# Performance work log

Hardware: AMD Instinct MI355X
Metric: run time of the kernel (lower is better)

Reference implementation:

```python
import jax, jax.numpy as jnp
import numpy as np

NP_, NB_, E_, BE_ = 10000, 30000, 300000, 8192
PIN, BIN, EA = 128, 128, 16
HID, GH = 64, 4
D, TH, L, NC, SEQ = 128, 4, 2, 10, 6


def _ln(x, g, b, eps=1e-5):
    m = x.mean(-1, keepdims=True)
    v = ((x - m) ** 2).mean(-1, keepdims=True)
    return (x - m) * jax.lax.rsqrt(v + eps) * g + b


def _seg_softmax(e, seg, n):
    m = jax.ops.segment_max(e, seg, num_segments=n)
    m = jnp.where(jnp.isfinite(m), m, 0.0)
    ex = jnp.exp(e - m[seg])
    s = jax.ops.segment_sum(ex, seg, num_segments=n)
    return ex / (s[seg] + 1e-16)


def _gatv2(xs, xd, es, ed, ea, Wl, bl, Wr, br, We, att, bias, n_dst):
    # PyG GATv2Conv, concat=False, add_self_loops=False, eval mode (no dropout)
    xl = (xs @ Wl + bl).reshape(-1, GH, HID)   # [Ns,H,C] source transform (message content)
    xr = (xd @ Wr + br).reshape(-1, GH, HID)   # [Nd,H,C] dest transform
    eh = (ea @ We).reshape(-1, GH, HID)        # [E,H,C] edge transform (no bias in PyG)
    msg = xl[es] + xr[ed] + eh                 # [E,H,C]
    score = jnp.einsum('ehc,hc->eh', jax.nn.leaky_relu(msg, 0.2), att)
    alpha = _seg_softmax(score, ed, n_dst)     # softmax over in-edges per dest node
    out = jax.ops.segment_sum(alpha[..., None] * xl[es], ed, num_segments=n_dst)
    return out.mean(axis=1) + bias             # concat=False -> mean over heads


def _mha(x, Wqkv, bqkv, Wo, bo):
    S, d = x.shape
    dh = d // TH
    q, k, v = jnp.split(x @ Wqkv + bqkv, 3, axis=-1)
    q = q.reshape(S, TH, dh).transpose(1, 0, 2)
    k = k.reshape(S, TH, dh).transpose(1, 0, 2)
    v = v.reshape(S, TH, dh).transpose(1, 0, 2)
    a = jax.nn.softmax(jnp.einsum('hqd,hkd->hqk', q, k) / jnp.sqrt(jnp.float32(dh)), axis=-1)
    o = jnp.einsum('hqk,hkd->hqd', a, v).transpose(1, 0, 2).reshape(S, d)
    return o @ Wo + bo


def _forward(pitcher_feat, batter_feat, edge_attr, history_states,
             Wp, bp, Wb, bb,
             rel_Wl, rel_bl, rel_Wr, rel_br, rel_We, rel_att, rel_bias,
             rev_Wl, rev_bl, rev_Wr, rev_br, rev_We, rev_att, rev_bias,
             Wgs, bgs, Wet, bet, pos,
             Wqkv, bqkv, Wo, bo, ln1g, ln1b, W1, b1, W2, b2, ln2g, ln2b,
             Wc1, bc1, Wc2, bc2,
             edge_src, edge_dst, edge_ids):
    gelu = lambda t: jax.nn.gelu(t, approximate=False)
    px = gelu(pitcher_feat @ Wp + bp)
    bx = gelu(batter_feat @ Wb + bb)
    # ('pitcher','faces','batter'): messages pitcher->batter, aggregated at batter nodes
    h_b = gelu(_gatv2(px, bx, edge_src, edge_dst, edge_attr,
                      rel_Wl, rel_bl, rel_Wr, rel_br, rel_We, rel_att, rel_bias, bx.shape[0]))
    # reversed relation: batter->pitcher, aggregated at pitcher nodes
    h_p = gelu(_gatv2(bx, px, edge_dst, edge_src, edge_attr,
                      rev_Wl, rev_bl, rev_Wr, rev_br, rev_We, rev_att, rev_bias, px.shape[0]))
    state = jnp.concatenate([h_p.mean(0), h_b.mean(0), edge_attr.mean(0)], -1) @ Wgs + bgs
    tok = jnp.concatenate([h_p[edge_src[edge_ids]], h_b[edge_dst[edge_ids]],
                           edge_attr[edge_ids]], -1) @ Wet + bet
    x = jnp.concatenate([history_states, state[None]], 0) + pos[:SEQ]
    for i in range(L):  # post-LN TransformerEncoderLayer, gelu activation, eval (no dropout)
        x = _ln(x + _mha(x, Wqkv[i], bqkv[i], Wo[i], bo[i]), ln1g[i], ln1b[i])
        f = gelu(x @ W1[i] + b1[i]) @ W2[i] + b2[i]
        x = _ln(x + f, ln2g[i], ln2b[i])
    ctx = x[-1]
    cat = jnp.concatenate([tok, jnp.broadcast_to(ctx, (tok.shape[0], D))], -1)
    return gelu(cat @ Wc1 + bc1) @ Wc2 + bc2


def setup_inputs() -> dict:
    key = jax.random.key(0)
    ks = iter(jax.random.split(key, 64))
    nrm = lambda shape, s: jax.random.normal(next(ks), shape, dtype=jnp.float32) * s
    d = {
        'pitcher_feat': nrm((NP_, PIN), 1.0),
        'batter_feat': nrm((NB_, BIN), 1.0),
        'edge_attr': nrm((E_, EA), 1.0),
        'history_states': nrm((SEQ - 1, D), 1.0),
        'Wp': nrm((PIN, HID), 0.05), 'bp': jnp.zeros((HID,), jnp.float32),
        'Wb': nrm((BIN, HID), 0.05), 'bb': jnp.zeros((HID,), jnp.float32),
    }
    for p in ('rel', 'rev'):
        d[p + '_Wl'] = nrm((HID, GH * HID), 0.05)
        d[p + '_bl'] = jnp.zeros((GH * HID,), jnp.float32)
        d[p + '_Wr'] = nrm((HID, GH * HID), 0.05)
        d[p + '_br'] = jnp.zeros((GH * HID,), jnp.float32)
        d[p + '_We'] = nrm((EA, GH * HID), 0.05)
        d[p + '_att'] = nrm((GH, HID), 0.05)
        d[p + '_bias'] = jnp.zeros((HID,), jnp.float32)
    cin = 2 * HID + EA
    d['Wgs'] = nrm((cin, D), 0.05); d['bgs'] = jnp.zeros((D,), jnp.float32)
    d['Wet'] = nrm((cin, D), 0.05); d['bet'] = jnp.zeros((D,), jnp.float32)
    d['pos'] = nrm((SEQ, D), 0.02)
    d['Wqkv'] = nrm((L, D, 3 * D), 0.05); d['bqkv'] = jnp.zeros((L, 3 * D), jnp.float32)
    d['Wo'] = nrm((L, D, D), 0.05); d['bo'] = jnp.zeros((L, D), jnp.float32)
    d['ln1g'] = jnp.ones((L, D), jnp.float32); d['ln1b'] = jnp.zeros((L, D), jnp.float32)
    d['W1'] = nrm((L, D, 4 * D), 0.05); d['b1'] = jnp.zeros((L, 4 * D), jnp.float32)
    d['W2'] = nrm((L, 4 * D, D), 0.05); d['b2'] = jnp.zeros((L, D), jnp.float32)
    d['ln2g'] = jnp.ones((L, D), jnp.float32); d['ln2b'] = jnp.zeros((L, D), jnp.float32)
    d['Wc1'] = nrm((2 * D, D), 0.05); d['bc1'] = jnp.zeros((D,), jnp.float32)
    d['Wc2'] = nrm((D, NC), 0.05); d['bc2'] = jnp.zeros((NC,), jnp.float32)
    d['edge_src'] = jax.random.randint(next(ks), (E_,), 0, NP_)
    d['edge_dst'] = jax.random.randint(next(ks), (E_,), 0, NB_)
    d['edge_ids'] = jax.random.randint(next(ks), (BE_,), 0, E_)
    return d


def reference(pitcher_feat, batter_feat, edge_attr, history_states,
              Wp, bp, Wb, bb,
              rel_Wl, rel_bl, rel_Wr, rel_br, rel_We, rel_att, rel_bias,
              rev_Wl, rev_bl, rev_Wr, rev_br, rev_We, rev_att, rev_bias,
              Wgs, bgs, Wet, bet, pos,
              Wqkv, bqkv, Wo, bo, ln1g, ln1b, W1, b1, W2, b2, ln2g, ln2b,
              Wc1, bc1, Wc2, bc2,
              edge_src, edge_dst, edge_ids):
    return _forward(pitcher_feat, batter_feat, edge_attr, history_states,
                    Wp, bp, Wb, bb,
                    rel_Wl, rel_bl, rel_Wr, rel_br, rel_We, rel_att, rel_bias,
                    rev_Wl, rev_bl, rev_Wr, rev_br, rev_We, rev_att, rev_bias,
                    Wgs, bgs, Wet, bet, pos,
                    Wqkv, bqkv, Wo, bo, ln1g, ln1b, W1, b1, W2, b2, ln2g, ln2b,
                    Wc1, bc1, Wc2, bc2,
                    edge_src, edge_dst, edge_ids)
```

## Files before the change

kernel.cpp:

```cpp
#include <hip/hip_runtime.h>
#include <math.h>

#define NP 10000
#define NB 30000
#define NEDGE 300000
#define BEDGE 8192
#define EAD 16
#define HID 64
#define GH 4
#define CW 256
#define DD 128
#define SEQ 6
#define NCLS 10
#define L 2

__device__ __forceinline__ float geluf(float x){
  return 0.5f * x * (1.0f + erff(x * 0.7071067811865475f));
}

__device__ __forceinline__ float b2f(unsigned short u){
  unsigned v = ((unsigned)u) << 16;
  return __int_as_float(v);
}
__device__ __forceinline__ unsigned short f2b(float f){
  unsigned x = __float_as_uint(f);
  unsigned r = x + 0x7FFF + ((x >> 16) & 1);
  return (unsigned short)(r >> 16);
}

typedef __attribute__((ext_vector_type(8))) short bf16x8;
typedef __attribute__((ext_vector_type(4))) float f32x4;

template<int KQ, int NTILES, bool A_F32, bool GELU>
__device__ __forceinline__
void mfma_gemm_body(int bid, const void* __restrict__ Av, const float* __restrict__ W,
                    const float* __restrict__ bias, unsigned short* __restrict__ out,
                    int M, unsigned short* __restrict__ sWt)
{
  constexpr int N  = NTILES * 16;
  constexpr int KP = KQ + 8;
  int t = threadIdx.x, w = t >> 6, l = t & 63;
  int c = l & 15, g = l >> 4;
  for (int idx = t; idx < KQ*N; idx += 256){
    int k = idx / N, n = idx - k*N;
    sWt[n*KP + k] = f2b(W[idx]);
  }
  __syncthreads();
  int rowbase = bid*64 + w*16;
  int arow = rowbase + c; if (arow > M-1) arow = M-1;
  f32x4 acc[NTILES] = {};
  #pragma unroll
  for (int ks = 0; ks < KQ/32; ++ks){
    int koff = ks*32 + g*8;
    bf16x8 a;
    if constexpr (A_F32){
      const float* Af = (const float*)Av + (size_t)arow*KQ + koff;
      float4 f0 = *(const float4*)Af;
      float4 f1 = *(const float4*)(Af + 4);
      a[0]=(short)f2b(f0.x); a[1]=(short)f2b(f0.y); a[2]=(short)f2b(f0.z); a[3]=(short)f2b(f0.w);
      a[4]=(short)f2b(f1.x); a[5]=(short)f2b(f1.y); a[6]=(short)f2b(f1.z); a[7]=(short)f2b(f1.w);
    } else {
      a = *(const bf16x8*)((const unsigned short*)Av + (size_t)arow*KQ + koff);
    }
    #pragma unroll
    for (int nt = 0; nt < NTILES; ++nt){
      bf16x8 b = *(const bf16x8*)&sWt[(nt*16 + c)*KP + koff];
      acc[nt] = __builtin_amdgcn_mfma_f32_16x16x32_bf16(a, b, acc[nt], 0, 0, 0);
    }
  }
  #pragma unroll
  for (int nt = 0; nt < NTILES; ++nt){
    #pragma unroll
    for (int j = 0; j < 4; ++j){
      int row = rowbase + g*4 + j;
      if (row < M){
        int col = nt*16 + c;
        float v = acc[nt][j] + bias[col];
        if (GELU) v = geluf(v);
        out[(size_t)row*N + col] = f2b(v);
      }
    }
  }
}

__global__ __launch_bounds__(256)
void k1_count_enc(const int* __restrict__ edst, const int* __restrict__ esrc,
                  int* __restrict__ degA, int* __restrict__ degB,
                  const float* __restrict__ pit, const float* __restrict__ Wp,
                  const float* __restrict__ bp, unsigned short* __restrict__ px,
                  const float* __restrict__ bat, const float* __restrict__ Wb,
                  const float* __restrict__ bb, unsigned short* __restrict__ bx,
                  int nbCount, int nbP)
{
  __shared__ unsigned short sWt[64*136];
  int b = blockIdx.x;
  if (b < nbCount){
    int i = b*256 + threadIdx.x;
    if (i < NEDGE){
      atomicAdd(&degA[edst[i]], 1);
      atomicAdd(&degB[esrc[i]], 1);
    }
  } else if (b < nbCount + nbP){
    mfma_gemm_body<128,4,true,true>(b - nbCount, pit, Wp, bp, px, NP, sWt);
  } else {
    mfma_gemm_body<128,4,true,true>(b - nbCount - nbP, bat, Wb, bb, bx, NB, sWt);
  }
}

__device__ void scan_dev(const int* __restrict__ deg, int* __restrict__ row_start,
                         int* __restrict__ cursor, int n){
  __shared__ int wsum[16];
  __shared__ int sbase;
  int t = threadIdx.x, w = t >> 6, l = t & 63;
  if (t == 0) sbase = 0;
  __syncthreads();
  for (int base = 0; base < n; base += 4096){
    int i = base + t*4;
    int4 v = make_int4(0,0,0,0);
    if (i < n) v = *(const int4*)(deg + i);
    int tsum = v.x + v.y + v.z + v.w;
    int x = tsum;
    #pragma unroll
    for (int off = 1; off < 64; off <<= 1){
      int y = __shfl_up(x, off);
      if (l >= off) x += y;
    }
    if (l == 63) wsum[w] = x;
    __syncthreads();
    int woff = 0, tot = 0;
    #pragma unroll
    for (int ww = 0; ww < 16; ++ww){
      int wv = wsum[ww];
      if (ww < w) woff += wv;
      tot += wv;
    }
    int excl = sbase + woff + x - tsum;
    if (i < n){
      int e1 = excl + v.x, e2 = excl + v.x + v.y, e3 = excl + v.x + v.y + v.z;
      row_start[i]   = excl; cursor[i]   = excl;
      row_start[i+1] = e1;   cursor[i+1] = e1;
      row_start[i+2] = e2;   cursor[i+2] = e2;
      row_start[i+3] = e3;   cursor[i+3] = e3;
    }
    __syncthreads();
    if (t == 0) sbase += tot;
    __syncthreads();
  }
  if (t == 0) row_start[n] = sbase;
}

__global__ __launch_bounds__(1024)
void scan2_kernel(const int* __restrict__ degA, int* __restrict__ rsA, int* __restrict__ curA, int nA,
                  const int* __restrict__ degB, int* __restrict__ rsB, int* __restrict__ curB, int nB,
                  float* __restrict__ mvec){
  if (blockIdx.x == 0){
    scan_dev(degA, rsA, curA, nA);
  } else {
    if (threadIdx.x < 144) mvec[threadIdx.x] = 0.f;
    scan_dev(degB, rsB, curB, nB);
  }
}

__global__ __launch_bounds__(256)
void k2_scatter_proj(const int* __restrict__ edst, const int* __restrict__ esrc,
                     int* __restrict__ curA, int* __restrict__ curB,
                     int2* __restrict__ csrA, int2* __restrict__ csrB,
                     const unsigned short* __restrict__ px, const unsigned short* __restrict__ bx,
                     const float* __restrict__ rel_Wl, const float* __restrict__ rel_bl,
                     const float* __restrict__ rel_Wr, const float* __restrict__ rel_br,
                     const float* __restrict__ rev_Wl, const float* __restrict__ rev_bl,
                     const float* __restrict__ rev_Wr, const float* __restrict__ rev_br,
                     unsigned short* __restrict__ xlA, unsigned short* __restrict__ xrA,
                     unsigned short* __restrict__ xlB, unsigned short* __restrict__ xrB,
                     int nbScat, int nbP, int nbB)
{
  __shared__ unsigned short sWt[256*72];
  int b = blockIdx.x;
  if (b < nbScat){
    int i = b*256 + threadIdx.x;
    if (i < NEDGE){
      int d = edst[i], s = esrc[i];
      int p = atomicAdd(&curA[d], 1);
      csrA[p] = make_int2(i, s);
      int q = atomicAdd(&curB[s], 1);
      csrB[q] = make_int2(i, d);
    }
  } else {
    b -= nbScat;
    if (b < nbP)               mfma_gemm_body<64,16,false,false>(b,            px, rel_Wl, rel_bl, xlA, NP, sWt);
    else if (b < nbP + nbB)    mfma_gemm_body<64,16,false,false>(b-nbP,        bx, rel_Wr, rel_br, xrA, NB, sWt);
    else if (b < nbP + 2*nbB)  mfma_gemm_body<64,16,false,false>(b-nbP-nbB,    bx, rev_Wl, rev_bl, xlB, NB, sWt);
    else                       mfma_gemm_body<64,16,false,false>(b-nbP-2*nbB,  px, rev_Wr, rev_br, xrB, NP, sWt);
  }
}

#define GAT_PAIR(X0, X1, EV0, EV1, V1OK, P0MASK)                             \
  {                                                                          \
    float x0 = b2f(X0.x), x1 = b2f(X0.y), x2 = b2f(X0.z), x3 = b2f(X0.w);    \
    float y0 = b2f(X1.x), y1 = b2f(X1.y), y2 = b2f(X1.z), y3 = b2f(X1.w);    \
    float h00 = x0 + r0, h01 = x1 + r1, h02 = x2 + r2, h03 = x3 + r3;        \
    float h10 = y0 + r0, h11 = y1 + r1, h12 = y2 + r2, h13 = y3 + r3;        \
    int ia0 = __float_as_int(EV0);                                           \
    int ia1 = __float_as_int(EV1);                                           \
    _Pragma("unroll")                                                        \
    for (int k = 0; k < EAD; ++k){                                           \
      float c0 = __int_as_float(__builtin_amdgcn_readlane(ia0, k));          \
      float c1 = __int_as_float(__builtin_amdgcn_readlane(ia1, k));          \
      float4 wv = *(const float4*)&sWe[k*CW + 4*l];                          \
      h00 = fmaf(c0, wv.x, h00); h01 = fmaf(c0, wv.y, h01);                  \
      h02 = fmaf(c0, wv.z, h02); h03 = fmaf(c0, wv.w, h03);                  \
      h10 = fmaf(c1, wv.x, h10); h11 = fmaf(c1, wv.y, h11);                  \
      h12 = fmaf(c1, wv.z, h12); h13 = fmaf(c1, wv.w, h13);                  \
    }                                                                        \
    h00 = (h00 > 0.f ? h00 : 0.2f*h00) * at.x;                               \
    h01 = (h01 > 0.f ? h01 : 0.2f*h01) * at.y;                               \
    h02 = (h02 > 0.f ? h02 : 0.2f*h02) * at.z;                               \
    h03 = (h03 > 0.f ? h03 : 0.2f*h03) * at.w;                               \
    h10 = (h10 > 0.f ? h10 : 0.2f*h10) * at.x;                               \
    h11 = (h11 > 0.f ? h11 : 0.2f*h11) * at.y;                               \
    h12 = (h12 > 0.f ? h12 : 0.2f*h12) * at.z;                               \
    h13 = (h13 > 0.f ? h13 : 0.2f*h13) * at.w;                               \
    float g0 = (h00 + h01) + (h02 + h03);                                    \
    float g1 = (h10 + h11) + (h12 + h13);                                    \
    _Pragma("unroll")                                                        \
    for (int off = 1; off < 16; off <<= 1){                                  \
      g0 += __shfl_xor(g0, off);                                             \
      g1 += __shfl_xor(g1, off);                                             \
    }                                                                        \
    float gm = (V1OK) ? fmaxf(g0, g1) : g0;                                  \
    float mn = fmaxf(m, gm);                                                 \
    float cc = __expf(m - mn);                                               \
    float p0 = __expf(g0 - mn);                                              \
    if (!(P0MASK)) p0 = 0.f;                                                 \
    float p1 = (V1OK) ? __expf(g1 - mn) : 0.f;                               \
    s  = fmaf(s, cc, p0 + p1);                                               \
    a0 = fmaf(a0, cc, fmaf(p1, y0, p0*x0));                                  \
    a1 = fmaf(a1, cc, fmaf(p1, y1, p0*x1));                                  \
    a2 = fmaf(a2, cc, fmaf(p1, y2, p0*x2));                                  \
    a3 = fmaf(a3, cc, fmaf(p1, y3, p0*x3));                                  \
    m = mn;                                                                  \
  }

__global__ __launch_bounds__(256)
void gat2_kernel(const unsigned short* __restrict__ xlA_, const unsigned short* __restrict__ xrA_,
                 const float* __restrict__ WeA, const float* __restrict__ attA,
                 const float* __restrict__ biasA, const int2* __restrict__ csrA_,
                 const int* __restrict__ rsA_, float* __restrict__ houtA,
                 const unsigned short* __restrict__ xlB_, const unsigned short* __restrict__ xrB_,
                 const float* __restrict__ WeB, const float* __restrict__ attB,
                 const float* __restrict__ biasB, const int2* __restrict__ csrB_,
                 const int* __restrict__ rsB_, float* __restrict__ houtB,
                 const float* __restrict__ ea, int gsplit)
{
  __shared__ float sWe[16*CW];
  bool isA = (int)blockIdx.x < gsplit;
  const unsigned short* xl = isA ? xlA_ : xlB_;
  const unsigned short* xr = isA ? xrA_ : xrB_;
  const float* We   = isA ? WeA   : WeB;
  const float* att  = isA ? attA  : attB;
  const float* bias = isA ? biasA : biasB;
  const int2* csr   = isA ? csrA_ : csrB_;
  const int* row_start = isA ? rsA_ : rsB_;
  float* hout = isA ? houtA : houtB;
  int ndst = isA ? NB : NP;
  int bid  = isA ? (int)blockIdx.x : (int)blockIdx.x - gsplit;
  int nblk = isA ? gsplit : (int)gridDim.x - gsplit;

  int t = threadIdx.x, l = t & 63;
  for (int i = t*4; i < 16*CW; i += 1024)
    *(float4*)&sWe[i] = *(const float4*)&We[i];
  __syncthreads();
  float4 at = *(const float4*)&att[4*l];
  float4 bi = *(const float4*)&bias[(l & 15)*4];
  int wid = bid*4 + (t >> 6);
  int nw = nblk*4;
  for (int d = wid; d < ndst; d += nw){
    ushort4 ru = *(const ushort4*)(xr + (size_t)d*CW + 4*l);
    float r0 = b2f(ru.x), r1 = b2f(ru.y), r2 = b2f(ru.z), r3 = b2f(ru.w);
    int rs = row_start[d], re = row_start[d+1];
    float m = -INFINITY, s = 0.f;
    float a0 = 0.f, a1 = 0.f, a2 = 0.f, a3 = 0.f;
    if (rs < re){
      int last = re - 1;
      #define CLMP(x) ((x) > last ? last : (x))
      int2 qA0 = csr[rs],         qA1 = csr[CLMP(rs+1)];
      int2 qB0 = csr[CLMP(rs+2)], qB1 = csr[CLMP(rs+3)];
      int2 nA0 = csr[CLMP(rs+4)], nA1 = csr[CLMP(rs+5)];
      int2 nB0 = csr[CLMP(rs+6)], nB1 = csr[CLMP(rs+7)];
      ushort4 xA0 = *(const ushort4*)(xl + (size_t)qA0.y*CW + 4*l);
      ushort4 xA1 = *(const ushort4*)(xl + (size_t)qA1.y*CW + 4*l);
      float  evA0 = ea[(size_t)qA0.x*EAD + (l & 15)];
      float  evA1 = ea[(size_t)qA1.x*EAD + (l & 15)];
      ushort4 xB0 = *(const ushort4*)(xl + (size_t)qB0.y*CW + 4*l);
      ushort4 xB1 = *(const ushort4*)(xl + (size_t)qB1.y*CW + 4*l);
      float  evB0 = ea[(size_t)qB0.x*EAD + (l & 15)];
      float  evB1 = ea[(size_t)qB1.x*EAD + (l & 15)];
      for (int i = rs; i < re; i += 4){
        int2 mA0 = csr[CLMP(i+8)],  mA1 = csr[CLMP(i+9)];
        int2 mB0 = csr[CLMP(i+10)], mB1 = csr[CLMP(i+11)];
        GAT_PAIR(xA0, xA1, evA0, evA1, (i+1 < re), true);
        xA0 = *(const ushort4*)(xl + (size_t)nA0.y*CW + 4*l);
        xA1 = *(const ushort4*)(xl + (size_t)nA1.y*CW + 4*l);
        evA0 = ea[(size_t)nA0.x*EAD + (l & 15)];
        evA1 = ea[(size_t)nA1.x*EAD + (l & 15)];
        nA0 = mA0; nA1 = mA1;
        GAT_PAIR(xB0, xB1, evB0, evB1, (i+3 < re), (i+2 < re));
        xB0 = *(const ushort4*)(xl + (size_t)nB0.y*CW + 4*l);
        xB1 = *(const ushort4*)(xl + (size_t)nB1.y*CW + 4*l);
        evB0 = ea[(size_t)nB0.x*EAD + (l & 15)];
        evB1 = ea[(size_t)nB1.x*EAD + (l & 15)];
        nB0 = mB0; nB1 = mB1;
      }
      #undef CLMP
    }
    float inv = 1.f / (s + 1e-16f);
    float v0 = a0*inv, v1 = a1*inv, v2 = a2*inv, v3 = a3*inv;
    v0 += __shfl_xor(v0, 16); v1 += __shfl_xor(v1, 16);
    v2 += __shfl_xor(v2, 16); v3 += __shfl_xor(v3, 16);
    v0 += __shfl_xor(v0, 32); v1 += __shfl_xor(v1, 32);
    v2 += __shfl_xor(v2, 32); v3 += __shfl_xor(v3, 32);
    if (l < 16){
      float4 o;
      o.x = geluf(v0*0.25f + bi.x);
      o.y = geluf(v1*0.25f + bi.y);
      o.z = geluf(v2*0.25f + bi.z);
      o.w = geluf(v3*0.25f + bi.w);
      *(float4*)(hout + (size_t)d*HID + 4*l) = o;
    }
  }
}

__device__ __forceinline__ void colsum_seg(int bid, int nb, const float4* __restrict__ in4,
                                           long total4, int n4, float* __restrict__ out,
                                           float scale, float* lds){
  int t = threadIdx.x, l = t & 63, w = t >> 6;
  long gid = (long)bid*256 + t;
  long stride = (long)nb*256;
  float4 acc = make_float4(0.f,0.f,0.f,0.f);
  for (long i = gid; i < total4; i += stride){
    float4 v = in4[i];
    acc.x += v.x; acc.y += v.y; acc.z += v.z; acc.w += v.w;
  }
  for (int off = n4; off < 64; off <<= 1){
    acc.x += __shfl_xor(acc.x, off);
    acc.y += __shfl_xor(acc.y, off);
    acc.z += __shfl_xor(acc.z, off);
    acc.w += __shfl_xor(acc.w, off);
  }
  if (l < n4) *(float4*)&lds[(w*n4 + l)*4] = acc;
  __syncthreads();
  if (t < n4*4){
    float sum = lds[t] + lds[n4*4 + t] + lds[2*n4*4 + t] + lds[3*n4*4 + t];
    atomicAdd(&out[t], sum * scale);
  }
  __syncthreads();
}

__device__ void colsum3_body(int bid, int nb, const float* __restrict__ hp,
                             const float* __restrict__ hb, const float* __restrict__ ea,
                             float* __restrict__ mvec){
  __shared__ float lds[4*16*4];
  colsum_seg(bid, nb, (const float4*)ea, (long)NEDGE*EAD/4, 4,  mvec+128, 1.f/NEDGE, lds);
  colsum_seg(bid, nb, (const float4*)hb, (long)NB*HID/4,    16, mvec+64,  1.f/NB,    lds);
  colsum_seg(bid, nb, (const float4*)hp, (long)NP*HID/4,    16, mvec,     1.f/NP,    lds);
}

__device__ void gemmcat_body(int bid, const float* __restrict__ hp, const float* __restrict__ hb,
                             const float* __restrict__ ea, const int* __restrict__ esrc,
                             const int* __restrict__ edst, const int* __restrict__ eids,
                             const float* __restrict__ W, const float* __restrict__ bias,
                             float* __restrict__ out)
{
  __shared__ float sAT[16][68];
  __shared__ float sB[16][68];
  __shared__ int sS[64], sD[64], sE[64];
  int t = threadIdx.x;
  int m0 = (bid >> 1)*64, n0 = (bid & 1)*64;
  if (t < 64){
    int e = eids[m0 + t];
    sS[t] = esrc[e]; sD[t] = edst[e]; sE[t] = e;
  }
  __syncthreads();
  int tr = t >> 4, tc = t & 15;
  float acc[4][4] = {};
  for (int k0 = 0; k0 < 144; k0 += 16){
    {
      int r = t >> 2, c = (t & 3) * 4;
      const float* src; int col = k0 + c;
      if (k0 < 64)       { src = hp + (size_t)sS[r]*HID; }
      else if (k0 < 128) { src = hb + (size_t)sD[r]*HID; col -= 64; }
      else               { src = ea + (size_t)sE[r]*EAD; col -= 128; }
      float4 va = *(const float4*)(src + col);
      sAT[c+0][r] = va.x; sAT[c+1][r] = va.y; sAT[c+2][r] = va.z; sAT[c+3][r] = va.w;
    }
    {
      int r = t >> 4, c = (t & 15) * 4;
      float4 vb = *(const float4*)(W + (size_t)(k0+r)*DD + n0 + c);
      *(float4*)&sB[r][c] = vb;
    }
    __syncthreads();
    #pragma unroll
    for (int k = 0; k < 16; ++k){
      float4 av = *(const float4*)&sAT[k][tr*4];
      float4 bv = *(const float4*)&sB[k][tc*4];
      acc[0][0] = fmaf(av.x, bv.x, acc[0][0]);
      acc[0][1] = fmaf(av.x, bv.y, acc[0][1]);
      acc[0][2] = fmaf(av.x, bv.z, acc[0][2]);
      acc[0][3] = fmaf(av.x, bv.w, acc[0][3]);
      acc[1][0] = fmaf(av.y, bv.x, acc[1][0]);
      acc[1][1] = fmaf(av.y, bv.y, acc[1][1]);
      acc[1][2] = fmaf(av.y, bv.z, acc[1][2]);
      acc[1][3] = fmaf(av.y, bv.w, acc[1][3]);
      acc[2][0] = fmaf(av.z, bv.x, acc[2][0]);
      acc[2][1] = fmaf(av.z, bv.y, acc[2][1]);
      acc[2][2] = fmaf(av.z, bv.z, acc[2][2]);
      acc[2][3] = fmaf(av.z, bv.w, acc[2][3]);
      acc[3][0] = fmaf(av.w, bv.x, acc[3][0]);
      acc[3][1] = fmaf(av.w, bv.y, acc[3][1]);
      acc[3][2] = fmaf(av.w, bv.z, acc[3][2]);
      acc[3][3] = fmaf(av.w, bv.w, acc[3][3]);
    }
    __syncthreads();
  }
  #pragma unroll
  for (int i = 0; i < 4; ++i){
    int gr = m0 + tr*4 + i;
    float4 v;
    v.x = acc[i][0] + bias[n0 + tc*4 + 0];
    v.y = acc[i][1] + bias[n0 + tc*4 + 1];
    v.z = acc[i][2] + bias[n0 + tc*4 + 2];
    v.w = acc[i][3] + bias[n0 + tc*4 + 3];
    *(float4*)(out + (size_t)gr*DD + n0 + tc*4) = v;
  }
}

__global__ __launch_bounds__(256)
void k3_colsum_gemmcat(const float* __restrict__ hp, const float* __restrict__ hb,
                       const float* __restrict__ ea, float* __restrict__ mvec,
                       const int* __restrict__ esrc, const int* __restrict__ edst,
                       const int* __restrict__ eids, const float* __restrict__ Wet,
                       const float* __restrict__ bet, float* __restrict__ tokb,
                       int nbCol)
{
  int b = blockIdx.x;
  if (b < nbCol) colsum3_body(b, nbCol, hp, hb, ea, mvec);
  else           gemmcat_body(b - nbCol, hp, hb, ea, esrc, edst, eids, Wet, bet, tokb);
}

template<int K, int N, int NC>
__device__ __forceinline__ void qstage(const float* __restrict__ x,
                                       const float* __restrict__ W,
                                       float (&a)[6][4], int q, int ch)
{
  constexpr int NQ = N/4;
  constexpr int KC = K/NC;
  const float4* wp = (const float4*)W + (size_t)(ch*KC)*NQ + q;
  const float* xb = x + ch*KC;
  #pragma unroll
  for (int s = 0; s < 6; ++s){ a[s][0]=0.f; a[s][1]=0.f; a[s][2]=0.f; a[s][3]=0.f; }
  #pragma unroll
  for (int j = 0; j < 4; ++j){
    int k4 = (j + ch) & 3;
    float4 wv0 = wp[(size_t)(k4*4+0)*NQ];
    float4 wv1 = wp[(size_t)(k4*4+1)*NQ];
    float4 wv2 = wp[(size_t)(k4*4+2)*NQ];
    float4 wv3 = wp[(size_t)(k4*4+3)*NQ];
    #pragma unroll
    for (int s = 0; s < 6; ++s){
      float4 xv = *(const float4*)&xb[s*K + k4*4];
      a[s][0]=fmaf(xv.x,wv0.x,a[s][0]); a[s][0]=fmaf(xv.y,wv1.x,a[s][0]);
      a[s][0]=fmaf(xv.z,wv2.x,a[s][0]); a[s][0]=fmaf(xv.w,wv3.x,a[s][0]);
      a[s][1]=fmaf(xv.x,wv0.y,a[s][1]); a[s][1]=fmaf(xv.y,wv1.y,a[s][1]);
      a[s][1]=fmaf(xv.z,wv2.y,a[s][1]); a[s][1]=fmaf(xv.w,wv3.y,a[s][1]);
      a[s][2]=fmaf(xv.x,wv0.z,a[s][2]); a[s][2]=fmaf(xv.y,wv1.z,a[s][2]);
      a[s][2]=fmaf(xv.z,wv2.z,a[s][2]); a[s][2]=fmaf(xv.w,wv3.z,a[s][2]);
      a[s][3]=fmaf(xv.x,wv0.w,a[s][3]); a[s][3]=fmaf(xv.y,wv1.w,a[s][3]);
      a[s][3]=fmaf(xv.z,wv2.w,a[s][3]); a[s][3]=fmaf(xv.w,wv3.w,a[s][3]);
    }
  }
  #pragma unroll
  for (int off = 1; off < NC; off <<= 1){
    #pragma unroll
    for (int s = 0; s < 6; ++s){
      a[s][0]+=__shfl_xor(a[s][0],off); a[s][1]+=__shfl_xor(a[s][1],off);
      a[s][2]+=__shfl_xor(a[s][2],off); a[s][3]+=__shfl_xor(a[s][3],off);
    }
  }
}

__global__ __launch_bounds__(512)
void xform_kernel(const float* __restrict__ hist, const float* __restrict__ mvec,
                  const float* __restrict__ Wgs, const float* __restrict__ bgs,
                  const float* __restrict__ pos,
                  const float* __restrict__ Wqkv, const float* __restrict__ bqkv,
                  const float* __restrict__ Wo, const float* __restrict__ bo,
                  const float* __restrict__ ln1g, const float* __restrict__ ln1b,
                  const float* __restrict__ W1, const float* __restrict__ b1,
                  const float* __restrict__ W2, const float* __restrict__ b2,
                  const float* __restrict__ ln2g, const float* __restrict__ ln2b,
                  const float* __restrict__ Wc1, const float* __restrict__ bc1,
                  float* __restrict__ bias2)
{
  __shared__ float sx[SEQ*DD];
  __shared__ float sq[SEQ*3*DD];
  __shared__ float sh[SEQ*512];
  __shared__ float st[SEQ*DD];
  __shared__ float sc[4][6][6];
  __shared__ float smean[SEQ], sinv[SEQ];
  __shared__ float smv[144];
  int t = threadIdx.x;

  for (int i = t; i < (SEQ-1)*DD; i += 512) sx[i] = hist[i] + pos[i];
  if (t < 144) smv[t] = mvec[t];
  __syncthreads();
  if (t < 256){
    int q = t >> 3, ch = t & 7;
    float a0=0.f,a1=0.f,a2=0.f,a3=0.f;
    #pragma unroll
    for (int kk = 0; kk < 18; ++kk){
      int k = ch*18 + kk;
      float4 wv = *(const float4*)&Wgs[k*DD + q*4];
      float xv = smv[k];
      a0=fmaf(xv,wv.x,a0); a1=fmaf(xv,wv.y,a1);
      a2=fmaf(xv,wv.z,a2); a3=fmaf(xv,wv.w,a3);
    }
    #pragma unroll
    for (int off = 1; off < 8; off <<= 1){
      a0+=__shfl_xor(a0,off); a1+=__shfl_xor(a1,off);
      a2+=__shfl_xor(a2,off); a3+=__shfl_xor(a3,off);
    }
    if (ch == 0){
      int n = q*4, base = (SEQ-1)*DD + n;
      sx[base+0]=a0+bgs[n+0]+pos[base+0];
      sx[base+1]=a1+bgs[n+1]+pos[base+1];
      sx[base+2]=a2+bgs[n+2]+pos[base+2];
      sx[base+3]=a3+bgs[n+3]+pos[base+3];
    }
  }
  __syncthreads();

  for (int lyr = 0; lyr < L; ++lyr){
    {
      const float* wq = Wqkv + (size_t)lyr*DD*3*DD;
      const float* bq = bqkv + lyr*3*DD;
      for (int u = t; u < 768; u += 512){
        int q = u >> 3, ch = u & 7;
        float a[6][4];
        qstage<128,384,8>(sx, wq, a, q, ch);
        if (ch == 0){
          int n = q*4;
          #pragma unroll
          for (int s = 0; s < 6; ++s){
            sq[s*384+n+0]=a[s][0]+bq[n+0];
            sq[s*384+n+1]=a[s][1]+bq[n+1];
            sq[s*384+n+2]=a[s][2]+bq[n+2];
            sq[s*384+n+3]=a[s][3]+bq[n+3];
          }
        }
      }
    }
    __syncthreads();
    if (t < 144){
      int h = t/36, r = t%36, qi = r/6, ki = r%6;
      float acc = 0.f;
      #pragma unroll
      for (int d2 = 0; d2 < 32; ++d2)
        acc = fmaf(sq[qi*384 + h*32 + d2], sq[ki*384 + 128 + h*32 + d2], acc);
      sc[h][qi][ki] = acc * 0.17677669529663687f;
    }
    __syncthreads();
    if (t < 24){
      int h = t/6, qi = t%6;
      float* row = sc[h][qi];
      float mx = row[0];
      #pragma unroll
      for (int k = 1; k < 6; ++k) mx = fmaxf(mx, row[k]);
      float sm = 0.f;
      #pragma unroll
      for (int k = 0; k < 6; ++k){ row[k] = __expf(row[k]-mx); sm += row[k]; }
      float inv = 1.f/sm;
      #pragma unroll
      for (int k = 0; k < 6; ++k) row[k] *= inv;
    }
    __syncthreads();
    for (int i = t; i < SEQ*DD; i += 512){
      int s = i >> 7, n = i & 127, h = n >> 5, d2 = n & 31;
      float acc = 0.f;
      #pragma unroll
      for (int ki = 0; ki < 6; ++ki)
        acc = fmaf(sc[h][s][ki], sq[ki*384 + 256 + h*32 + d2], acc);
      st[i] = acc;
    }
    __syncthreads();
    if (t < 256){
      int q = t >> 3, ch = t & 7;
      float a[6][4];
      qstage<128,128,8>(st, Wo + (size_t)lyr*DD*DD, a, q, ch);
      if (ch == 0){
        int n = q*4;
        const float* bop = bo + lyr*DD;
        #pragma unroll
        for (int s = 0; s < 6; ++s){
          sh[s*128+n+0]=a[s][0]+bop[n+0]+sx[s*128+n+0];
          sh[s*128+n+1]=a[s][1]+bop[n+1]+sx[s*128+n+1];
          sh[s*128+n+2]=a[s][2]+bop[n+2]+sx[s*128+n+2];
          sh[s*128+n+3]=a[s][3]+bop[n+3]+sx[s*128+n+3];
        }
      }
    }
    __syncthreads();
    {
      int w = t >> 6, lw = t & 63;
      if (w < SEQ){
        float v0 = sh[w*DD + lw], v1 = sh[w*DD + 64 + lw];
        float sm = v0 + v1;
        #pragma unroll
        for (int off = 1; off < 64; off <<= 1) sm += __shfl_xor(sm, off);
        float mean = sm * 0.0078125f;
        float d0 = v0-mean, d1 = v1-mean;
        float qv = d0*d0 + d1*d1;
        #pragma unroll
        for (int off = 1; off < 64; off <<= 1) qv += __shfl_xor(qv, off);
        if (lw == 0){ smean[w] = mean; sinv[w] = rsqrtf(qv*0.0078125f + 1e-5f); }
      }
    }
    __syncthreads();
    {
      const float* g = ln1g + lyr*DD; const float* be = ln1b + lyr*DD;
      for (int i = t; i < SEQ*DD; i += 512){
        int s = i >> 7, n = i & 127;
        sx[i] = (sh[i]-smean[s])*sinv[s]*g[n] + be[n];
      }
    }
    __syncthreads();
    {
      const float* w1 = W1 + (size_t)lyr*DD*512;
      const float* b1p = b1 + lyr*512;
      for (int u = t; u < 1024; u += 512){
        int q = u >> 3, ch = u & 7;
        float a[6][4];
        qstage<128,512,8>(sx, w1, a, q, ch);
        if (ch == 0){
          int n = q*4;
          #pragma unroll
          for (int s = 0; s < 6; ++s){
            sh[s*512+n+0]=geluf(a[s][0]+b1p[n+0]);
            sh[s*512+n+1]=geluf(a[s][1]+b1p[n+1]);
            sh[s*512+n+2]=geluf(a[s][2]+b1p[n+2]);
            sh[s*512+n+3]=geluf(a[s][3]+b1p[n+3]);
          }
        }
      }
    }
    __syncthreads();
    {
      const float* w2 = W2 + (size_t)lyr*512*DD;
      const float* b2p = b2 + lyr*DD;
      for (int u = t; u < 1024; u += 512){
        int q = u >> 5, ch = u & 31;
        float a[6][4];
        qstage<512,128,32>(sh, w2, a, q, ch);
        if (ch == 0){
          int n = q*4;
          #pragma unroll
          for (int s = 0; s < 6; ++s){
            st[s*128+n+0]=a[s][0]+b2p[n+0]+sx[s*128+n+0];
            st[s*128+n+1]=a[s][1]+b2p[n+1]+sx[s*128+n+1];
            st[s*128+n+2]=a[s][2]+b2p[n+2]+sx[s*128+n+2];
            st[s*128+n+3]=a[s][3]+b2p[n+3]+sx[s*128+n+3];
          }
        }
      }
    }
    __syncthreads();
    {
      int w = t >> 6, lw = t & 63;
      if (w < SEQ){
        float v0 = st[w*DD + lw], v1 = st[w*DD + 64 + lw];
        float sm = v0 + v1;
        #pragma unroll
        for (int off = 1; off < 64; off <<= 1) sm += __shfl_xor(sm, off);
        float mean = sm * 0.0078125f;
        float d0 = v0-mean, d1 = v1-mean;
        float qv = d0*d0 + d1*d1;
        #pragma unroll
        for (int off = 1; off < 64; off <<= 1) qv += __shfl_xor(qv, off);
        if (lw == 0){ smean[w] = mean; sinv[w] = rsqrtf(qv*0.0078125f + 1e-5f); }
      }
    }
    __syncthreads();
    {
      const float* g = ln2g + lyr*DD; const float* be = ln2b + lyr*DD;
      for (int i = t; i < SEQ*DD; i += 512){
        int s = i >> 7, n = i & 127;
        sx[i] = (st[i]-smean[s])*sinv[s]*g[n] + be[n];
      }
    }
    __syncthreads();
  }
  if (t < 256){
    int q = t >> 3, ch = t & 7;
    const float4* wp = (const float4*)(Wc1 + (size_t)DD*DD) + (size_t)(ch*16)*32 + q;
    const float* xb = &sx[(SEQ-1)*DD + ch*16];
    float a0=0.f,a1=0.f,a2=0.f,a3=0.f;
    #pragma unroll
    for (int kk = 0; kk < 16; ++kk){
      float4 wv = wp[(size_t)kk*32];
      float xv = xb[kk];
      a0=fmaf(xv,wv.x,a0); a1=fmaf(xv,wv.y,a1);
      a2=fmaf(xv,wv.z,a2); a3=fmaf(xv,wv.w,a3);
    }
    #pragma unroll
    for (int off = 1; off < 8; off <<= 1){
      a0+=__shfl_xor(a0,off); a1+=__shfl_xor(a1,off);
      a2+=__shfl_xor(a2,off); a3+=__shfl_xor(a3,off);
    }
    if (ch == 0){
      int n = q*4;
      bias2[n+0]=a0+bc1[n+0];
      bias2[n+1]=a1+bc1[n+1];
      bias2[n+2]=a2+bc1[n+2];
      bias2[n+3]=a3+bc1[n+3];
    }
  }
}

template<bool GELU>
__global__ __launch_bounds__(256)
void gemm64_kernel(const float* __restrict__ A, const float* __restrict__ W,
                   const float* __restrict__ bias, float* __restrict__ out,
                   int M, int K, int N)
{
  __shared__ float sAT[16][68];
  __shared__ float sB[16][68];
  int t = threadIdx.x;
  int m0 = blockIdx.x * 64, n0 = blockIdx.y * 64;
  int tr = t >> 4, tc = t & 15;
  float acc[4][4] = {};
  for (int k0 = 0; k0 < K; k0 += 16){
    {
      int r = t >> 2, c = (t & 3) * 4;
      int gr = m0 + r;
      float4 va = make_float4(0.f,0.f,0.f,0.f);
      if (gr < M) va = *(const float4*)(A + (size_t)gr*K + k0 + c);
      sAT[c+0][r] = va.x; sAT[c+1][r] = va.y; sAT[c+2][r] = va.z; sAT[c+3][r] = va.w;
    }
    {
      int r = t >> 4, c = (t & 15) * 4;
      float4 vb = *(const float4*)(W + (size_t)(k0+r)*N + n0 + c);
      *(float4*)&sB[r][c] = vb;
    }
    __syncthreads();
    #pragma unroll
    for (int k = 0; k < 16; ++k){
      float4 av = *(const float4*)&sAT[k][tr*4];
      float4 bv = *(const float4*)&sB[k][tc*4];
      acc[0][0] = fmaf(av.x, bv.x, acc[0][0]);
      acc[0][1] = fmaf(av.x, bv.y, acc[0][1]);
      acc[0][2] = fmaf(av.x, bv.z, acc[0][2]);
      acc[0][3] = fmaf(av.x, bv.w, acc[0][3]);
      acc[1][0] = fmaf(av.y, bv.x, acc[1][0]);
      acc[1][1] = fmaf(av.y, bv.y, acc[1][1]);
      acc[1][2] = fmaf(av.y, bv.z, acc[1][2]);
      acc[1][3] = fmaf(av.y, bv.w, acc[1][3]);
      acc[2][0] = fmaf(av.z, bv.x, acc[2][0]);
      acc[2][1] = fmaf(av.z, bv.y, acc[2][1]);
      acc[2][2] = fmaf(av.z, bv.z, acc[2][2]);
      acc[2][3] = fmaf(av.z, bv.w, acc[2][3]);
      acc[3][0] = fmaf(av.w, bv.x, acc[3][0]);
      acc[3][1] = fmaf(av.w, bv.y, acc[3][1]);
      acc[3][2] = fmaf(av.w, bv.z, acc[3][2]);
      acc[3][3] = fmaf(av.w, bv.w, acc[3][3]);
    }
    __syncthreads();
  }
  #pragma unroll
  for (int i = 0; i < 4; ++i){
    int gr = m0 + tr*4 + i;
    if (gr < M){
      float4 v;
      v.x = acc[i][0] + bias[n0 + tc*4 + 0];
      v.y = acc[i][1] + bias[n0 + tc*4 + 1];
      v.z = acc[i][2] + bias[n0 + tc*4 + 2];
      v.w = acc[i][3] + bias[n0 + tc*4 + 3];
      if (GELU){ v.x = geluf(v.x); v.y = geluf(v.y); v.z = geluf(v.z); v.w = geluf(v.w); }
      *(float4*)(out + (size_t)gr*N + n0 + tc*4) = v;
    }
  }
}

__global__ void head2_kernel(const float* __restrict__ hid, const float* __restrict__ Wc2,
                             const float* __restrict__ bc2, float* __restrict__ out){
  int i = blockIdx.x*blockDim.x + threadIdx.x;
  if (i >= BEDGE*16) return;
  int tok = i >> 4, c = i & 15;
  if (c < NCLS){
    float acc = bc2[c];
    const float4* hr4 = (const float4*)(hid + (size_t)tok*DD);
    #pragma unroll 8
    for (int k4 = 0; k4 < 32; ++k4){
      float4 hv = hr4[k4];
      acc = fmaf(hv.x, Wc2[(4*k4+0)*NCLS + c], acc);
      acc = fmaf(hv.y, Wc2[(4*k4+1)*NCLS + c], acc);
      acc = fmaf(hv.z, Wc2[(4*k4+2)*NCLS + c], acc);
      acc = fmaf(hv.w, Wc2[(4*k4+3)*NCLS + c], acc);
    }
    out[tok*NCLS + c] = acc;
  }
}

extern "C" void kernel_launch(void* const* d_in, const int* in_sizes, int n_in,
                              void* d_out, int out_size, void* d_ws, size_t ws_size,
                              hipStream_t stream){
  (void)in_sizes; (void)n_in; (void)out_size; (void)ws_size;
  const float* pitcher = (const float*)d_in[0];
  const float* batter  = (const float*)d_in[1];
  const float* eattr   = (const float*)d_in[2];
  const float* hist    = (const float*)d_in[3];
  const float* Wp = (const float*)d_in[4];
  const float* bp = (const float*)d_in[5];
  const float* Wb = (const float*)d_in[6];
  const float* bb = (const float*)d_in[7];
  const float* rel_Wl  = (const float*)d_in[8];
  const float* rel_bl  = (const float*)d_in[9];
  const float* rel_Wr  = (const float*)d_in[10];
  const float* rel_br  = (const float*)d_in[11];
  const float* rel_We  = (const float*)d_in[12];
  const float* rel_att = (const float*)d_in[13];
  const float* rel_bias= (const float*)d_in[14];
  const float* rev_Wl  = (const float*)d_in[15];
  const float* rev_bl  = (const float*)d_in[16];
  const float* rev_Wr  = (const float*)d_in[17];
  const float* rev_br  = (const float*)d_in[18];
  const float* rev_We  = (const float*)d_in[19];
  const float* rev_att = (const float*)d_in[20];
  const float* rev_bias= (const float*)d_in[21];
  const float* Wgs = (const float*)d_in[22];
  const float* bgs = (const float*)d_in[23];
  const float* Wet = (const float*)d_in[24];
  const float* bet = (const float*)d_in[25];
  const float* pos = (const float*)d_in[26];
  const float* Wqkv= (const float*)d_in[27];
  const float* bqkv= (const float*)d_in[28];
  const float* Wo  = (const float*)d_in[29];
  const float* bo  = (const float*)d_in[30];
  const float* ln1g= (const float*)d_in[31];
  const float* ln1b= (const float*)d_in[32];
  const float* W1  = (const float*)d_in[33];
  const float* b1  = (const float*)d_in[34];
  const float* W2  = (const float*)d_in[35];
  const float* b2  = (const float*)d_in[36];
  const float* ln2g= (const float*)d_in[37];
  const float* ln2b= (const float*)d_in[38];
  const float* Wc1 = (const float*)d_in[39];
  const float* bc1 = (const float*)d_in[40];
  const float* Wc2 = (const float*)d_in[41];
  const float* bc2 = (const float*)d_in[42];
  const int* esrc = (const int*)d_in[43];
  const int* edst = (const int*)d_in[44];
  const int* eids = (const int*)d_in[45];

  char* w = (char*)d_ws;
  size_t off = 0;
  auto alloc = [&](size_t bytes)->void*{
    void* p = (void*)(w + off);
    off += (bytes + 255) & ~(size_t)255;
    return p;
  };
  unsigned short* px_bf  = (unsigned short*)alloc((size_t)NP*HID*2);
  unsigned short* bx_bf  = (unsigned short*)alloc((size_t)NB*HID*2);
  float*          hp     = (float*)alloc((size_t)NP*HID*4);
  float*          hb     = (float*)alloc((size_t)NB*HID*4);
  unsigned short* xlA    = (unsigned short*)alloc((size_t)NP*CW*2);
  unsigned short* xrA    = (unsigned short*)alloc((size_t)NB*CW*2);
  unsigned short* xlB    = (unsigned short*)alloc((size_t)NB*CW*2);
  unsigned short* xrB    = (unsigned short*)alloc((size_t)NP*CW*2);
  int*            degAB  = (int*)alloc((size_t)(NB+NP)*4);
  int*            degA   = degAB;
  int*            degB   = degAB + NB;
  int*            rowstA = (int*)alloc((size_t)(NB+1)*4);
  int*            rowstB = (int*)alloc((size_t)(NP+1)*4);
  int*            cursA  = (int*)alloc((size_t)NB*4);
  int*            cursB  = (int*)alloc((size_t)NP*4);
  int2*           csrA   = (int2*)alloc((size_t)NEDGE*8);
  int2*           csrB   = (int2*)alloc((size_t)NEDGE*8);
  float*          mvec   = (float*)alloc(144*4);
  float*          bias2  = (float*)alloc(DD*4);
  float*          tokb   = (float*)xlA;
  float*          hid    = (float*)xrA;

  const int nbCount = (NEDGE + 255)/256;
  const int nbP = (NP + 63)/64;
  const int nbB = (NB + 63)/64;

  hipMemsetAsync(degAB, 0, (size_t)(NB+NP)*4, stream);
  k1_count_enc<<<nbCount + nbP + nbB, 256, 0, stream>>>(
      edst, esrc, degA, degB,
      pitcher, Wp, bp, px_bf, batter, Wb, bb, bx_bf, nbCount, nbP);

  scan2_kernel<<<2, 1024, 0, stream>>>(degA, rowstA, cursA, NB,
                                       degB, rowstB, cursB, NP, mvec);

  k2_scatter_proj<<<nbCount + 2*nbP + 2*nbB, 256, 0, stream>>>(
      edst, esrc, cursA, cursB, csrA, csrB, px_bf, bx_bf,
      rel_Wl, rel_bl, rel_Wr, rel_br, rev_Wl, rev_bl, rev_Wr, rev_br,
      xlA, xrA, xlB, xrB, nbCount, nbP, nbB);

  gat2_kernel<<<4096, 256, 0, stream>>>(
      xlA, xrA, rel_We, rel_att, rel_bias, csrA, rowstA, hb,
      xlB, xrB, rev_We, rev_att, rev_bias, csrB, rowstB, hp,
      eattr, 2048);

  k3_colsum_gemmcat<<<512, 256, 0, stream>>>(
      hp, hb, eattr, mvec, esrc, edst, eids, Wet, bet, tokb, 256);

  xform_kernel<<<1, 512, 0, stream>>>(
      hist, mvec, Wgs, bgs, pos, Wqkv, bqkv, Wo, bo, ln1g, ln1b,
      W1, b1, W2, b2, ln2g, ln2b, Wc1, bc1, bias2);

  gemm64_kernel<true><<<dim3(BEDGE/64,2), 256, 0, stream>>>(tokb, Wc1, bias2, hid, BEDGE, DD, DD);
  head2_kernel<<<(BEDGE*16+255)/256, 256, 0, stream>>>(hid, Wc2, bc2, (float*)d_out);
}
```

Baseline: 419.2 us.

## Prefetch transformer weights into registers and remap thread work in single-block transformer kernel

```diff
diff --git a/kernel.cpp b/kernel.cpp
--- a/kernel.cpp
+++ b/kernel.cpp
@@ -448,34 +448,41 @@
 }
 
 template<int K, int N, int NC>
-__device__ __forceinline__ void qstage(const float* __restrict__ x,
-                                       const float* __restrict__ W,
-                                       float (&a)[6][4], int q, int ch)
+__device__ __forceinline__ void qstageF(const float* __restrict__ x,
+                                        const float* __restrict__ W,
+                                        float (&a)[6][4], int q, int ch)
 {
   constexpr int NQ = N/4;
   constexpr int KC = K/NC;
+  constexpr int J  = KC/4;
   const float4* wp = (const float4*)W + (size_t)(ch*KC)*NQ + q;
   const float* xb = x + ch*KC;
+  float4 wv[KC];
+  int kx[J];
+  #pragma unroll
+  for (int j = 0; j < J; ++j){
+    int k4 = (j + ch) & (J-1);
+    kx[j] = k4;
+    wv[j*4+0] = wp[(size_t)(k4*4+0)*NQ];
+    wv[j*4+1] = wp[(size_t)(k4*4+1)*NQ];
+    wv[j*4+2] = wp[(size_t)(k4*4+2)*NQ];
+    wv[j*4+3] = wp[(size_t)(k4*4+3)*NQ];
+  }
   #pragma unroll
   for (int s = 0; s < 6; ++s){ a[s][0]=0.f; a[s][1]=0.f; a[s][2]=0.f; a[s][3]=0.f; }
   #pragma unroll
-  for (int j = 0; j < 4; ++j){
-    int k4 = (j + ch) & 3;
-    float4 wv0 = wp[(size_t)(k4*4+0)*NQ];
-    float4 wv1 = wp[(size_t)(k4*4+1)*NQ];
-    float4 wv2 = wp[(size_t)(k4*4+2)*NQ];
-    float4 wv3 = wp[(size_t)(k4*4+3)*NQ];
+  for (int j = 0; j < J; ++j){
     #pragma unroll
     for (int s = 0; s < 6; ++s){
-      float4 xv = *(const float4*)&xb[s*K + k4*4];
-      a[s][0]=fmaf(xv.x,wv0.x,a[s][0]); a[s][0]=fmaf(xv.y,wv1.x,a[s][0]);
-      a[s][0]=fmaf(xv.z,wv2.x,a[s][0]); a[s][0]=fmaf(xv.w,wv3.x,a[s][0]);
-      a[s][1]=fmaf(xv.x,wv0.y,a[s][1]); a[s][1]=fmaf(xv.y,wv1.y,a[s][1]);
-      a[s][1]=fmaf(xv.z,wv2.y,a[s][1]); a[s][1]=fmaf(xv.w,wv3.y,a[s][1]);
-      a[s][2]=fmaf(xv.x,wv0.z,a[s][2]); a[s][2]=fmaf(xv.y,wv1.z,a[s][2]);
-      a[s][2]=fmaf(xv.z,wv2.z,a[s][2]); a[s][2]=fmaf(xv.w,wv3.z,a[s][2]);
-      a[s][3]=fmaf(xv.x,wv0.w,a[s][3]); a[s][3]=fmaf(xv.y,wv1.w,a[s][3]);
-      a[s][3]=fmaf(xv.z,wv2.w,a[s][3]); a[s][3]=fmaf(xv.w,wv3.w,a[s][3]);
+      float4 xv = *(const float4*)&xb[s*K + kx[j]*4];
+      a[s][0]=fmaf(xv.x,wv[j*4+0].x,a[s][0]); a[s][0]=fmaf(xv.y,wv[j*4+1].x,a[s][0]);
+      a[s][0]=fmaf(xv.z,wv[j*4+2].x,a[s][0]); a[s][0]=fmaf(xv.w,wv[j*4+3].x,a[s][0]);
+      a[s][1]=fmaf(xv.x,wv[j*4+0].y,a[s][1]); a[s][1]=fmaf(xv.y,wv[j*4+1].y,a[s][1]);
+      a[s][1]=fmaf(xv.z,wv[j*4+2].y,a[s][1]); a[s][1]=fmaf(xv.w,wv[j*4+3].y,a[s][1]);
+      a[s][2]=fmaf(xv.x,wv[j*4+0].z,a[s][2]); a[s][2]=fmaf(xv.y,wv[j*4+1].z,a[s][2]);
+      a[s][2]=fmaf(xv.z,wv[j*4+2].z,a[s][2]); a[s][2]=fmaf(xv.w,wv[j*4+3].z,a[s][2]);
+      a[s][3]=fmaf(xv.x,wv[j*4+0].w,a[s][3]); a[s][3]=fmaf(xv.y,wv[j*4+1].w,a[s][3]);
+      a[s][3]=fmaf(xv.z,wv[j*4+2].w,a[s][3]); a[s][3]=fmaf(xv.w,wv[j*4+3].w,a[s][3]);
     }
   }
   #pragma unroll
@@ -506,7 +513,6 @@
   __shared__ float sh[SEQ*512];
   __shared__ float st[SEQ*DD];
   __shared__ float sc[4][6][6];
-  __shared__ float smean[SEQ], sinv[SEQ];
   __shared__ float smv[144];
   int t = threadIdx.x;
 
@@ -515,14 +521,16 @@
   __syncthreads();
   if (t < 256){
     int q = t >> 3, ch = t & 7;
+    float4 wv[18];
+    #pragma unroll
+    for (int kk = 0; kk < 18; ++kk)
+      wv[kk] = *(const float4*)&Wgs[(ch*18+kk)*DD + q*4];
     float a0=0.f,a1=0.f,a2=0.f,a3=0.f;
     #pragma unroll
     for (int kk = 0; kk < 18; ++kk){
-      int k = ch*18 + kk;
-      float4 wv = *(const float4*)&Wgs[k*DD + q*4];
-      float xv = smv[k];
-      a0=fmaf(xv,wv.x,a0); a1=fmaf(xv,wv.y,a1);
-      a2=fmaf(xv,wv.z,a2); a3=fmaf(xv,wv.w,a3);
+      float xv = smv[ch*18+kk];
+      a0=fmaf(xv,wv[kk].x,a0); a1=fmaf(xv,wv[kk].y,a1);
+      a2=fmaf(xv,wv[kk].z,a2); a3=fmaf(xv,wv[kk].w,a3);
     }
     #pragma unroll
     for (int off = 1; off < 8; off <<= 1){
@@ -540,22 +548,20 @@
   __syncthreads();
 
   for (int lyr = 0; lyr < L; ++lyr){
-    {
+    if (t < 384){
+      int q = t >> 2, ch = t & 3;
       const float* wq = Wqkv + (size_t)lyr*DD*3*DD;
       const float* bq = bqkv + lyr*3*DD;
-      for (int u = t; u < 768; u += 512){
-        int q = u >> 3, ch = u & 7;
-        float a[6][4];
-        qstage<128,384,8>(sx, wq, a, q, ch);
-        if (ch == 0){
-          int n = q*4;
-          #pragma unroll
-          for (int s = 0; s < 6; ++s){
-            sq[s*384+n+0]=a[s][0]+bq[n+0];
-            sq[s*384+n+1]=a[s][1]+bq[n+1];
-            sq[s*384+n+2]=a[s][2]+bq[n+2];
-            sq[s*384+n+3]=a[s][3]+bq[n+3];
-          }
+      float a[6][4];
+      qstageF<128,384,4>(sx, wq, a, q, ch);
+      if (ch == 0){
+        int n = q*4;
+        #pragma unroll
+        for (int s = 0; s < 6; ++s){
+          sq[s*384+n+0]=a[s][0]+bq[n+0];
+          sq[s*384+n+1]=a[s][1]+bq[n+1];
+          sq[s*384+n+2]=a[s][2]+bq[n+2];
+          sq[s*384+n+3]=a[s][3]+bq[n+3];
         }
       }
     }
@@ -592,10 +598,10 @@
       st[i] = acc;
     }
     __syncthreads();
-    if (t < 256){
-      int q = t >> 3, ch = t & 7;
+    {
+      int q = t >> 4, ch = t & 15;
       float a[6][4];
-      qstage<128,128,8>(st, Wo + (size_t)lyr*DD*DD, a, q, ch);
+      qstageF<128,128,16>(st, Wo + (size_t)lyr*DD*DD, a, q, ch);
       if (ch == 0){
         int n = q*4;
         const float* bop = bo + lyr*DD;
@@ -612,6 +618,7 @@
     {
       int w = t >> 6, lw = t & 63;
       if (w < SEQ){
+        const float* g = ln1g + lyr*DD; const float* be = ln1b + lyr*DD;
         float v0 = sh[w*DD + lw], v1 = sh[w*DD + 64 + lw];
         float sm = v0 + v1;
         #pragma unroll
@@ -621,54 +628,44 @@
         float qv = d0*d0 + d1*d1;
         #pragma unroll
         for (int off = 1; off < 64; off <<= 1) qv += __shfl_xor(qv, off);
-        if (lw == 0){ smean[w] = mean; sinv[w] = rsqrtf(qv*0.0078125f + 1e-5f); }
+        float inv = rsqrtf(qv*0.0078125f + 1e-5f);
+        sx[w*DD + lw]      = d0*inv*g[lw] + be[lw];
+        sx[w*DD + 64 + lw] = d1*inv*g[64+lw] + be[64+lw];
       }
     }
     __syncthreads();
     {
-      const float* g = ln1g + lyr*DD; const float* be = ln1b + lyr*DD;
-      for (int i = t; i < SEQ*DD; i += 512){
-        int s = i >> 7, n = i & 127;
-        sx[i] = (sh[i]-smean[s])*sinv[s]*g[n] + be[n];
-      }
-    }
-    __syncthreads();
-    {
+      int q = t >> 2, ch = t & 3;
       const float* w1 = W1 + (size_t)lyr*DD*512;
       const float* b1p = b1 + lyr*512;
-      for (int u = t; u < 1024; u += 512){
-        int q = u >> 3, ch = u & 7;
-        float a[6][4];
-        qstage<128,512,8>(sx, w1, a, q, ch);
-        if (ch == 0){
-          int n = q*4;
-          #pragma unroll
-          for (int s = 0; s < 6; ++s){
-            sh[s*512+n+0]=geluf(a[s][0]+b1p[n+0]);
-            sh[s*512+n+1]=geluf(a[s][1]+b1p[n+1]);
-            sh[s*512+n+2]=geluf(a[s][2]+b1p[n+2]);
-            sh[s*512+n+3]=geluf(a[s][3]+b1p[n+3]);
-          }
+      float a[6][4];
+      qstageF<128,512,4>(sx, w1, a, q, ch);
+      if (ch == 0){
+        int n = q*4;
+        #pragma unroll
+        for (int s = 0; s < 6; ++s){
+          sh[s*512+n+0]=geluf(a[s][0]+b1p[n+0]);
+          sh[s*512+n+1]=geluf(a[s][1]+b1p[n+1]);
+          sh[s*512+n+2]=geluf(a[s][2]+b1p[n+2]);
+          sh[s*512+n+3]=geluf(a[s][3]+b1p[n+3]);
         }
       }
     }
     __syncthreads();
     {
+      int q = t >> 4, ch = t & 15;
       const float* w2 = W2 + (size_t)lyr*512*DD;
       const float* b2p = b2 + lyr*DD;
-      for (int u = t; u < 1024; u += 512){
-        int q = u >> 5, ch = u & 31;
-        float a[6][4];
-        qstage<512,128,32>(sh, w2, a, q, ch);
-        if (ch == 0){
-          int n = q*4;
-          #pragma unroll
-          for (int s = 0; s < 6; ++s){
-            st[s*128+n+0]=a[s][0]+b2p[n+0]+sx[s*128+n+0];
-            st[s*128+n+1]=a[s][1]+b2p[n+1]+sx[s*128+n+1];
-            st[s*128+n+2]=a[s][2]+b2p[n+2]+sx[s*128+n+2];
-            st[s*128+n+3]=a[s][3]+b2p[n+3]+sx[s*128+n+3];
-          }
+      float a[6][4];
+      qstageF<512,128,16>(sh, w2, a, q, ch);
+      if (ch == 0){
+        int n = q*4;
+        #pragma unroll
+        for (int s = 0; s < 6; ++s){
+          st[s*128+n+0]=a[s][0]+b2p[n+0]+sx[s*128+n+0];
+          st[s*128+n+1]=a[s][1]+b2p[n+1]+sx[s*128+n+1];
+          st[s*128+n+2]=a[s][2]+b2p[n+2]+sx[s*128+n+2];
+          st[s*128+n+3]=a[s][3]+b2p[n+3]+sx[s*128+n+3];
         }
       }
     }
@@ -676,6 +673,7 @@
     {
       int w = t >> 6, lw = t & 63;
       if (w < SEQ){
+        const float* g = ln2g + lyr*DD; const float* be = ln2b + lyr*DD;
         float v0 = st[w*DD + lw], v1 = st[w*DD + 64 + lw];
         float sm = v0 + v1;
         #pragma unroll
@@ -685,15 +683,9 @@
         float qv = d0*d0 + d1*d1;
         #pragma unroll
         for (int off = 1; off < 64; off <<= 1) qv += __shfl_xor(qv, off);
-        if (lw == 0){ smean[w] = mean; sinv[w] = rsqrtf(qv*0.0078125f + 1e-5f); }
-      }
-    }
-    __syncthreads();
-    {
-      const float* g = ln2g + lyr*DD; const float* be = ln2b + lyr*DD;
-      for (int i = t; i < SEQ*DD; i += 512){
-        int s = i >> 7, n = i & 127;
-        sx[i] = (st[i]-smean[s])*sinv[s]*g[n] + be[n];
+        float inv = rsqrtf(qv*0.0078125f + 1e-5f);
+        sx[w*DD + lw]      = d0*inv*g[lw] + be[lw];
+        sx[w*DD + 64 + lw] = d1*inv*g[64+lw] + be[64+lw];
       }
     }
     __syncthreads();
@@ -702,13 +694,29 @@
     int q = t >> 3, ch = t & 7;
     const float4* wp = (const float4*)(Wc1 + (size_t)DD*DD) + (size_t)(ch*16)*32 + q;
     const float* xb = &sx[(SEQ-1)*DD + ch*16];
+    float4 wv[16];
+    int kx[4];
+    #pragma unroll
+    for (int j = 0; j < 4; ++j){
+      int k4 = (j + ch) & 3;
+      kx[j] = k4;
+      wv[j*4+0] = wp[(size_t)(k4*4+0)*32];
+      wv[j*4+1] = wp[(size_t)(k4*4+1)*32];
+      wv[j*4+2] = wp[(size_t)(k4*4+2)*32];
+      wv[j*4+3] = wp[(size_t)(k4*4+3)*32];
+    }
     float a0=0.f,a1=0.f,a2=0.f,a3=0.f;
     #pragma unroll
-    for (int kk = 0; kk < 16; ++kk){
-      float4 wv = wp[(size_t)kk*32];
-      float xv = xb[kk];
-      a0=fmaf(xv,wv.x,a0); a1=fmaf(xv,wv.y,a1);
-      a2=fmaf(xv,wv.z,a2); a3=fmaf(xv,wv.w,a3);
+    for (int j = 0; j < 4; ++j){
+      float4 xv = *(const float4*)&xb[kx[j]*4];
+      a0=fmaf(xv.x,wv[j*4+0].x,a0); a0=fmaf(xv.y,wv[j*4+1].x,a0);
+      a0=fmaf(xv.z,wv[j*4+2].x,a0); a0=fmaf(xv.w,wv[j*4+3].x,a0);
+      a1=fmaf(xv.x,wv[j*4+0].y,a1); a1=fmaf(xv.y,wv[j*4+1].y,a1);
+      a1=fmaf(xv.z,wv[j*4+2].y,a1); a1=fmaf(xv.w,wv[j*4+3].y,a1);
+      a2=fmaf(xv.x,wv[j*4+0].z,a2); a2=fmaf(xv.y,wv[j*4+1].z,a2);
+      a2=fmaf(xv.z,wv[j*4+2].z,a2); a2=fmaf(xv.w,wv[j*4+3].z,a2);
+      a3=fmaf(xv.x,wv[j*4+0].w,a3); a3=fmaf(xv.y,wv[j*4+1].w,a3);
+      a3=fmaf(xv.z,wv[j*4+2].w,a3); a3=fmaf(xv.w,wv[j*4+3].w,a3);
     }
     #pragma unroll
     for (int off = 1; off < 8; off <<= 1){
```

New measurement: 387.3 us. -7.6%, faster.
